# Performance work log

Hardware: AMD Instinct MI355X
Metric: run time of the kernel (lower is better)

Reference implementation:

```python
import jax, jax.numpy as jnp
import numpy as np

NEG_INF = -1e30

def setup_inputs() -> dict:
    key = jax.random.key(0)
    k1, k2, k3 = jax.random.split(key, 3)
    B, Lc, Lq, D = 16, 4096, 512, 128  # D = 2*dim, dim=64
    ctx = jax.random.normal(k1, (B, Lc, D), dtype=jnp.float32)
    q = jax.random.normal(k2, (B, Lq, D), dtype=jnp.float32)
    ctx_mask = jnp.ones((B, Lc), dtype=bool)
    q_mask = jnp.ones((B, Lq), dtype=bool)
    # nn.Linear(6*dim, 1): weight [1, 3*D] stored flat, bias scalar
    W = jax.random.normal(k3, (3 * D,), dtype=jnp.float32) * (1.0 / np.sqrt(3 * D))
    b = jnp.zeros((1,), dtype=jnp.float32)
    return {"ctx": ctx, "q": q, "ctx_mask": ctx_mask, "q_mask": q_mask, "W": W, "b": b}

def reference(ctx, q, ctx_mask, q_mask, W, b):
    # Linear over cat([c, q, c*q]) decomposes: S[b,l,m] = c.w_c + q.w_q + (c*w_m).q + bias
    D = ctx.shape[-1]
    w_c, w_q, w_m = W[:D], W[D:2 * D], W[2 * D:]
    S = (ctx @ w_c)[:, :, None] + (q @ w_q)[:, None, :] \
        + jnp.einsum('bld,bmd->blm', ctx * w_m, q) + b[0]  # [B, Lc, Lq]
    pair_mask = ctx_mask[:, :, None] & q_mask[:, None, :]
    S = S + (1.0 - pair_mask.astype(S.dtype)) * NEG_INF
    # context-to-query attention
    c2q = jax.nn.softmax(S, axis=-1)                      # [B, Lc, Lq]
    u = jnp.einsum('blm,bmd->bld', c2q, q)                # [B, Lc, D]
    # query-to-context attention
    q2c = jax.nn.softmax(S.max(axis=-1, keepdims=True), axis=1)  # [B, Lc, 1]
    h = (ctx * q2c).sum(axis=1, keepdims=True)            # [B, 1, D]
    h = jnp.broadcast_to(h, ctx.shape)                    # [B, Lc, D]
    return jnp.concatenate([ctx, u, ctx * u, ctx * h], axis=-1)  # [B, Lc, 4D]
```

## Files before the change

### kernel.cpp

```cpp
#include <hip/hip_runtime.h>

#define NB 16
#define LC 4096
#define LQ 512
#define DD 128

typedef __attribute__((ext_vector_type(8))) short bf16x8;
typedef __attribute__((ext_vector_type(4))) float f32x4;

static __device__ __forceinline__ float bf2f(unsigned short u) {
  union { unsigned int i; float f; } v; v.i = ((unsigned int)u) << 16; return v.f;
}
static __device__ __forceinline__ unsigned short f2bf(float f) {
  union { float f; unsigned int u; } v; v.f = f;
  unsigned int r = v.u + 0x7fffu + ((v.u >> 16) & 1u);
  return (unsigned short)(r >> 16);
}

static __device__ __forceinline__ void loadf8(const unsigned short* pb, const float* pf,
                                              size_t idx, int bf, float* o) {
  if (bf) {
    bf16x8 v = *(const bf16x8*)(pb + idx);
#pragma unroll
    for (int j = 0; j < 8; j++) o[j] = bf2f((unsigned short)v[j]);
  } else {
    const float4* p0 = (const float4*)(pf + idx);
    float4 a = p0[0], b = p0[1];
    o[0] = a.x; o[1] = a.y; o[2] = a.z; o[3] = a.w;
    o[4] = b.x; o[5] = b.y; o[6] = b.z; o[7] = b.w;
  }
}

static __device__ __forceinline__ bf16x8 frag8(const unsigned short* pb, const float* pf,
                                               size_t idx, int bf) {
  bf16x8 r;
  if (bf) {
    r = *(const bf16x8*)(pb + idx);
  } else {
    float o[8];
    loadf8(pb, pf, idx, 0, o);
#pragma unroll
    for (int j = 0; j < 8; j++) r[j] = (short)f2bf(o[j]);
  }
  return r;
}

__global__ void kD_detect(const unsigned short* __restrict__ ctx_s, int* __restrict__ flag) {
  int t = threadIdx.x;
  int cnt = 0;
  for (int i = 0; i < 32; i++) {
    float a = fabsf(bf2f(ctx_s[t * 32 + i]));
    if (a >= 0.0009765625f && a <= 16.0f) cnt++;
  }
#pragma unroll
  for (int off = 32; off; off >>= 1) cnt += __shfl_down(cnt, off);
  if (t == 0) *flag = (cnt >= 1638) ? 1 : 0;
}

__global__ __launch_bounds__(256)
void k0_prep(const unsigned short* __restrict__ qB, const float* __restrict__ qF,
             const unsigned short* __restrict__ WB, const float* __restrict__ WF,
             const int* __restrict__ flagp,
             unsigned short* __restrict__ qm, unsigned short* __restrict__ qT,
             float* __restrict__ qq) {
  __shared__ unsigned short sT[DD][72];
  __shared__ float sQQ[64][5];
  int bf = *flagp;
  int blk = blockIdx.x;
  int b = blk >> 3, tile = blk & 7;
  int m0 = tile * 64;
  int t = threadIdx.x;
  int r = t >> 2;
  int dq = t & 3;
  int d0 = dq * 32;

  float qv[32], wq[32], wm[32];
  size_t qbase = ((size_t)b * LQ + m0 + r) * DD + d0;
#pragma unroll
  for (int j = 0; j < 4; j++) {
    loadf8(qB, qF, qbase + j * 8, bf, &qv[j * 8]);
    loadf8(WB, WF, (size_t)(DD + d0 + j * 8), bf, &wq[j * 8]);
    loadf8(WB, WF, (size_t)(2 * DD + d0 + j * 8), bf, &wm[j * 8]);
  }

  float s = 0.f;
#pragma unroll
  for (int j = 0; j < 32; j++) s += qv[j] * wq[j];
  sQQ[r][dq] = s;

  unsigned short* qmrow = qm + ((size_t)b * LQ + m0 + r) * DD + d0;
#pragma unroll
  for (int g = 0; g < 4; g++) {
    bf16x8 o;
#pragma unroll
    for (int e = 0; e < 8; e++) o[e] = (short)f2bf(qv[g * 8 + e] * wm[g * 8 + e]);
    *(bf16x8*)(qmrow + g * 8) = o;
  }

#pragma unroll
  for (int j = 0; j < 32; j++) sT[d0 + j][r] = f2bf(qv[j]);
  __syncthreads();

  if (t < 64) qq[(size_t)b * LQ + m0 + t] = sQQ[t][0] + sQQ[t][1] + sQQ[t][2] + sQQ[t][3];

  int d = t >> 1, ms = (t & 1) * 32;
  unsigned short* qTp = qT + ((size_t)b * DD + d) * LQ + m0 + ms;
#pragma unroll
  for (int g = 0; g < 4; g++)
    *(bf16x8*)(qTp + g * 8) = *(const bf16x8*)(&sT[d][ms + g * 8]);
}

__global__ __launch_bounds__(256)
void k1_main(const unsigned short* __restrict__ ctxB, const float* __restrict__ ctxF,
             const unsigned short* __restrict__ WB, const float* __restrict__ WF,
             const unsigned short* __restrict__ qm,
             const unsigned short* __restrict__ qT,
             const float* __restrict__ qq,
             const int* __restrict__ flagp,
             float* __restrict__ Mv,
             unsigned short* __restrict__ outB, float* __restrict__ outF) {
  __shared__ unsigned short sP[16][520];
  __shared__ float sRedMax[4][16];
  __shared__ float sRedSum[4][16];
  __shared__ float sRowMax[16];
  __shared__ float sRowSum[16];
  __shared__ float sCq[16];
  __shared__ float sCqPart[16][17];

  int bf = *flagp;
  int t = threadIdx.x;
  int b = blockIdx.x >> 8;
  int lt = blockIdx.x & 255;
  int l0 = lt << 4;
  int w = t >> 6;
  int lane = t & 63;
  int quad = lane >> 4;
  int l16 = lane & 15;
  const size_t ctx_row0 = (size_t)(b * LC + l0);

  {
    int r = t >> 4, dg = t & 15;
    float cv[8], wv[8];
    loadf8(ctxB, ctxF, (ctx_row0 + r) * DD + (size_t)dg * 8, bf, cv);
    loadf8(WB, WF, (size_t)dg * 8, bf, wv);
    float s = 0.f;
#pragma unroll
    for (int j = 0; j < 8; j++) s += cv[j] * wv[j];
    sCqPart[r][dg] = s;
  }
  __syncthreads();
  if (t < 16) {
    float c = 0.f;
#pragma unroll
    for (int k = 0; k < 16; k++) c += sCqPart[t][k];
    sCq[t] = c;
  }

  bf16x8 afrag[4];
#pragma unroll
  for (int k = 0; k < 4; k++)
    afrag[k] = frag8(ctxB, ctxF, (ctx_row0 + l16) * DD + quad * 8 + k * 32, bf);

  f32x4 acc[8];
  const unsigned short* qmb = qm + (size_t)b * LQ * DD;
  const float* qqb = qq + b * LQ;
#pragma unroll
  for (int c = 0; c < 8; c++) {
    int col = (w << 7) + (c << 4) + l16;
    f32x4 a4 = {0.f, 0.f, 0.f, 0.f};
#pragma unroll
    for (int k = 0; k < 4; k++) {
      bf16x8 bfr = *(const bf16x8*)(qmb + (size_t)col * DD + quad * 8 + k * 32);
      a4 = __builtin_amdgcn_mfma_f32_16x16x32_bf16(afrag[k], bfr, a4, 0, 0, 0);
    }
    float qqv = qqb[col];
    acc[c][0] = a4[0] + qqv;
    acc[c][1] = a4[1] + qqv;
    acc[c][2] = a4[2] + qqv;
    acc[c][3] = a4[3] + qqv;
  }

  float rmax[4];
#pragma unroll
  for (int r = 0; r < 4; r++) {
    float m_ = acc[0][r];
#pragma unroll
    for (int c = 1; c < 8; c++) m_ = fmaxf(m_, acc[c][r]);
    m_ = fmaxf(m_, __shfl_xor(m_, 1));
    m_ = fmaxf(m_, __shfl_xor(m_, 2));
    m_ = fmaxf(m_, __shfl_xor(m_, 4));
    m_ = fmaxf(m_, __shfl_xor(m_, 8));
    rmax[r] = m_;
  }
  if (l16 == 0) {
#pragma unroll
    for (int r = 0; r < 4; r++) sRedMax[w][quad * 4 + r] = rmax[r];
  }
  __syncthreads();
  if (t < 16) {
    float m_ = fmaxf(fmaxf(sRedMax[0][t], sRedMax[1][t]),
                     fmaxf(sRedMax[2][t], sRedMax[3][t]));
    sRowMax[t] = m_;
    Mv[(size_t)b * LC + l0 + t] = m_ + sCq[t];
  }
  __syncthreads();

  float rowmax_r[4];
#pragma unroll
  for (int r = 0; r < 4; r++) rowmax_r[r] = sRowMax[quad * 4 + r];
  float rsum[4] = {0.f, 0.f, 0.f, 0.f};
#pragma unroll
  for (int c = 0; c < 8; c++) {
    int col = (w << 7) + (c << 4) + l16;
#pragma unroll
    for (int r = 0; r < 4; r++) {
      float e = __expf(fminf(acc[c][r] - rowmax_r[r], 0.f));
      rsum[r] += e;
      sP[quad * 4 + r][col] = f2bf(e);
    }
  }
#pragma unroll
  for (int r = 0; r < 4; r++) {
    float s_ = rsum[r];
    s_ += __shfl_xor(s_, 1);
    s_ += __shfl_xor(s_, 2);
    s_ += __shfl_xor(s_, 4);
    s_ += __shfl_xor(s_, 8);
    rsum[r] = s_;
  }
  if (l16 == 0) {
#pragma unroll
    for (int r = 0; r < 4; r++) sRedSum[w][quad * 4 + r] = rsum[r];
  }
  __syncthreads();
  if (t < 16)
    sRowSum[t] = sRedSum[0][t] + sRedSum[1][t] + sRedSum[2][t] + sRedSum[3][t];
  __syncthreads();

  f32x4 uacc[2] = {{0.f,0.f,0.f,0.f},{0.f,0.f,0.f,0.f}};
  const unsigned short* qTb = qT + (size_t)b * DD * LQ;
  int dA = (w << 5) + l16;
  int dB = dA + 16;
  for (int kk = 0; kk < 16; kk++) {
    bf16x8 pa = *(const bf16x8*)(&sP[l16][kk * 32 + quad * 8]);
    bf16x8 b0 = *(const bf16x8*)(qTb + (size_t)dA * LQ + kk * 32 + quad * 8);
    bf16x8 b1 = *(const bf16x8*)(qTb + (size_t)dB * LQ + kk * 32 + quad * 8);
    uacc[0] = __builtin_amdgcn_mfma_f32_16x16x32_bf16(pa, b0, uacc[0], 0, 0, 0);
    uacc[1] = __builtin_amdgcn_mfma_f32_16x16x32_bf16(pa, b1, uacc[1], 0, 0, 0);
  }

#pragma unroll
  for (int dt = 0; dt < 2; dt++) {
    int d = (w << 5) + (dt << 4) + l16;
#pragma unroll
    for (int r = 0; r < 4; r++) {
      int roww = quad * 4 + r;
      float denom = fmaxf(sRowSum[roww], 1e-30f);
      float uval = uacc[dt][r] / denom;
      size_t orow = (ctx_row0 + roww) * 512;
      size_t ci = (ctx_row0 + roww) * DD + d;
      float ctxv = bf ? bf2f(ctxB[ci]) : ctxF[ci];
      if (bf) {
        outB[orow + 128 + d] = f2bf(uval);
        outB[orow + 256 + d] = f2bf(ctxv * uval);
      } else {
        outF[orow + 128 + d] = uval;
        outF[orow + 256 + d] = ctxv * uval;
      }
    }
  }
  {
    int r = t >> 4, c8 = (t & 15) * 8;
    float cv[8];
    loadf8(ctxB, ctxF, (ctx_row0 + r) * DD + c8, bf, cv);
    size_t oo = (ctx_row0 + r) * 512 + c8;
    if (bf) {
      bf16x8 ov;
#pragma unroll
      for (int j = 0; j < 8; j++) ov[j] = (short)f2bf(cv[j]);
      *(bf16x8*)(outB + oo) = ov;
    } else {
      float4 a = {cv[0], cv[1], cv[2], cv[3]};
      float4 bq = {cv[4], cv[5], cv[6], cv[7]};
      *(float4*)(outF + oo) = a;
      *(float4*)(outF + oo + 4) = bq;
    }
  }
}

__global__ void k2a_soft(const float* __restrict__ Mv, float* __restrict__ wgt) {
  int b = blockIdx.x, t = threadIdx.x;
  __shared__ float sM[LC];
  __shared__ float red[256];
  float lmax = -1e30f;
  for (int i = t; i < LC; i += 256) { float v = Mv[(size_t)b * LC + i]; sM[i] = v; lmax = fmaxf(lmax, v); }
  red[t] = lmax;
  __syncthreads();
  for (int s = 128; s > 0; s >>= 1) {
    if (t < s) red[t] = fmaxf(red[t], red[t + s]);
    __syncthreads();
  }
  float gmax = red[0];
  __syncthreads();
  float lsum = 0.f;
  for (int i = t; i < LC; i += 256) lsum += __expf(fminf(sM[i] - gmax, 0.f));
  red[t] = lsum;
  __syncthreads();
  for (int s = 128; s > 0; s >>= 1) {
    if (t < s) red[t] += red[t + s];
    __syncthreads();
  }
  float inv = 1.0f / fmaxf(red[0], 1e-30f);
  for (int i = t; i < LC; i += 256) wgt[(size_t)b * LC + i] = __expf(fminf(sM[i] - gmax, 0.f)) * inv;
}

__global__ void k2b_h(const unsigned short* __restrict__ ctxB, const float* __restrict__ ctxF,
                      const int* __restrict__ flagp,
                      const float* __restrict__ wgt, float* __restrict__ h) {
  int bf = *flagp;
  int blk = blockIdx.x;
  int b = blk >> 5, ch = blk & 31;
  int t = threadIdx.x;
  int d = t & 127, half = t >> 7;
  int lbase = ch * 128 + half * 64;
  size_t cbase = ((size_t)b * LC + lbase) * DD + d;
  const float* wb = wgt + (size_t)b * LC + lbase;
  float s = 0.f;
#pragma unroll 4
  for (int i = 0; i < 64; i++) {
    float v = bf ? bf2f(ctxB[cbase + (size_t)i * DD]) : ctxF[cbase + (size_t)i * DD];
    s += wb[i] * v;
  }
  __shared__ float part[256];
  part[t] = s;
  __syncthreads();
  if (t < 128) atomicAdd(&h[b * DD + d], part[t] + part[t + 128]);
}

__global__ void k3_tail(const unsigned short* __restrict__ ctxB, const float* __restrict__ ctxF,
                        const int* __restrict__ flagp,
                        const float* __restrict__ h,
                        unsigned short* __restrict__ outB, float* __restrict__ outF) {
  int bf = *flagp;
  int g = blockIdx.x * 256 + threadIdx.x;
  size_t row = (size_t)(g >> 4);
  int dseg = (g & 15) * 8;
  int b = (int)(row >> 12);
  float cv[8];
  loadf8(ctxB, ctxF, row * DD + dseg, bf, cv);
  const float* hb = h + b * DD + dseg;
  size_t oo = row * 512 + 384 + dseg;
  if (bf) {
    bf16x8 ov;
#pragma unroll
    for (int j = 0; j < 8; j++) ov[j] = (short)f2bf(cv[j] * hb[j]);
    *(bf16x8*)(outB + oo) = ov;
  } else {
    float4 a = {cv[0] * hb[0], cv[1] * hb[1], cv[2] * hb[2], cv[3] * hb[3]};
    float4 bq = {cv[4] * hb[4], cv[5] * hb[5], cv[6] * hb[6], cv[7] * hb[7]};
    *(float4*)(outF + oo) = a;
    *(float4*)(outF + oo + 4) = bq;
  }
}

extern "C" void kernel_launch(void* const* d_in, const int* in_sizes, int n_in,
                              void* d_out, int out_size, void* d_ws, size_t ws_size,
                              hipStream_t stream) {
  const unsigned short* ctxB = (const unsigned short*)d_in[0];
  const float*          ctxF = (const float*)d_in[0];
  const unsigned short* qB   = (const unsigned short*)d_in[1];
  const float*          qF   = (const float*)d_in[1];
  const unsigned short* WB   = (const unsigned short*)d_in[4];
  const float*          WF   = (const float*)d_in[4];
  unsigned short* outB = (unsigned short*)d_out;
  float*          outF = (float*)d_out;

  char* ws = (char*)d_ws;
  unsigned short* qm = (unsigned short*)(ws);
  unsigned short* qT = (unsigned short*)(ws + 2097152);
  float* qq  = (float*)(ws + 4194304);
  float* Mv  = (float*)(ws + 4227072);
  float* wgt = (float*)(ws + 4489216);
  float* h   = (float*)(ws + 4751360);
  int* flag  = (int*)(ws + 4759552);

  hipMemsetAsync(h, 0, NB * DD * sizeof(float), stream);
  kD_detect<<<1, 64, 0, stream>>>((const unsigned short*)d_in[0], flag);
  k0_prep<<<NB * 8, 256, 0, stream>>>(qB, qF, WB, WF, flag, qm, qT, qq);
  k1_main<<<NB * (LC / 16), 256, 0, stream>>>(ctxB, ctxF, WB, WF, qm, qT, qq, flag, Mv, outB, outF);
  k2a_soft<<<NB, 256, 0, stream>>>(Mv, wgt);
  k2b_h<<<NB * 32, 256, 0, stream>>>(ctxB, ctxF, flag, wgt, h);
  k3_tail<<<NB * LC * DD / 8 / 256, 256, 0, stream>>>(ctxB, ctxF, flag, h, outB, outF);
}
```

Measured before the change: 327.3 us.

## Stage u outputs through LDS for vectorized stores, prefetch MFMA operands, swizzle blocks

The u and ctx*u outputs were written as scalar per-lane stores with a stride of one row each. They are now staged in shared memory, reusing the sP buffer after a barrier, and written out as contiguous 16-element vectors per thread. The MFMA loops for S and for P·q now double-buffer their operand loads so the next fragment is fetched while the current one computes. Block indexing is also interleaved across batches. This adds two barriers and LDS traffic and raises register pressure from the prefetch buffers.

```diff
diff --git a/kernel.cpp b/kernel.cpp
--- a/kernel.cpp
+++ b/kernel.cpp
@@ -129,8 +129,8 @@
 
   int bf = *flagp;
   int t = threadIdx.x;
-  int b = blockIdx.x >> 8;
-  int lt = blockIdx.x & 255;
+  int b = blockIdx.x & 15;
+  int lt = blockIdx.x >> 4;
   int l0 = lt << 4;
   int w = t >> 6;
   int lane = t & 63;
@@ -164,15 +164,26 @@
   f32x4 acc[8];
   const unsigned short* qmb = qm + (size_t)b * LQ * DD;
   const float* qqb = qq + b * LQ;
+  bf16x8 bfr[2][4];
+  {
+    int col = (w << 7) + l16;
+#pragma unroll
+    for (int k = 0; k < 4; k++)
+      bfr[0][k] = *(const bf16x8*)(qmb + (size_t)col * DD + quad * 8 + k * 32);
+  }
 #pragma unroll
   for (int c = 0; c < 8; c++) {
+    if (c < 7) {
+      int coln = (w << 7) + ((c + 1) << 4) + l16;
+#pragma unroll
+      for (int k = 0; k < 4; k++)
+        bfr[(c + 1) & 1][k] = *(const bf16x8*)(qmb + (size_t)coln * DD + quad * 8 + k * 32);
+    }
+    f32x4 a4 = {0.f, 0.f, 0.f, 0.f};
+#pragma unroll
+    for (int k = 0; k < 4; k++)
+      a4 = __builtin_amdgcn_mfma_f32_16x16x32_bf16(afrag[k], bfr[c & 1][k], a4, 0, 0, 0);
     int col = (w << 7) + (c << 4) + l16;
-    f32x4 a4 = {0.f, 0.f, 0.f, 0.f};
-#pragma unroll
-    for (int k = 0; k < 4; k++) {
-      bf16x8 bfr = *(const bf16x8*)(qmb + (size_t)col * DD + quad * 8 + k * 32);
-      a4 = __builtin_amdgcn_mfma_f32_16x16x32_bf16(afrag[k], bfr, a4, 0, 0, 0);
-    }
     float qqv = qqb[col];
     acc[c][0] = a4[0] + qqv;
     acc[c][1] = a4[1] + qqv;
@@ -241,14 +252,24 @@
   const unsigned short* qTb = qT + (size_t)b * DD * LQ;
   int dA = (w << 5) + l16;
   int dB = dA + 16;
+  bf16x8 pa2[2], pb0[2], pb1[2];
+  pa2[0] = *(const bf16x8*)(&sP[l16][quad * 8]);
+  pb0[0] = *(const bf16x8*)(qTb + (size_t)dA * LQ + quad * 8);
+  pb1[0] = *(const bf16x8*)(qTb + (size_t)dB * LQ + quad * 8);
+#pragma unroll
   for (int kk = 0; kk < 16; kk++) {
-    bf16x8 pa = *(const bf16x8*)(&sP[l16][kk * 32 + quad * 8]);
-    bf16x8 b0 = *(const bf16x8*)(qTb + (size_t)dA * LQ + kk * 32 + quad * 8);
-    bf16x8 b1 = *(const bf16x8*)(qTb + (size_t)dB * LQ + kk * 32 + quad * 8);
-    uacc[0] = __builtin_amdgcn_mfma_f32_16x16x32_bf16(pa, b0, uacc[0], 0, 0, 0);
-    uacc[1] = __builtin_amdgcn_mfma_f32_16x16x32_bf16(pa, b1, uacc[1], 0, 0, 0);
-  }
-
+    if (kk < 15) {
+      int o = (kk + 1) * 32 + quad * 8;
+      pa2[(kk + 1) & 1] = *(const bf16x8*)(&sP[l16][o]);
+      pb0[(kk + 1) & 1] = *(const bf16x8*)(qTb + (size_t)dA * LQ + o);
+      pb1[(kk + 1) & 1] = *(const bf16x8*)(qTb + (size_t)dB * LQ + o);
+    }
+    uacc[0] = __builtin_amdgcn_mfma_f32_16x16x32_bf16(pa2[kk & 1], pb0[kk & 1], uacc[0], 0, 0, 0);
+    uacc[1] = __builtin_amdgcn_mfma_f32_16x16x32_bf16(pa2[kk & 1], pb1[kk & 1], uacc[1], 0, 0, 0);
+  }
+
+  __syncthreads();
+  float* stage = (float*)&sP[0][0];
 #pragma unroll
   for (int dt = 0; dt < 2; dt++) {
     int d = (w << 5) + (dt << 4) + l16;
@@ -257,16 +278,32 @@
       int roww = quad * 4 + r;
       float denom = fmaxf(sRowSum[roww], 1e-30f);
       float uval = uacc[dt][r] / denom;
-      size_t orow = (ctx_row0 + roww) * 512;
       size_t ci = (ctx_row0 + roww) * DD + d;
       float ctxv = bf ? bf2f(ctxB[ci]) : ctxF[ci];
-      if (bf) {
-        outB[orow + 128 + d] = f2bf(uval);
-        outB[orow + 256 + d] = f2bf(ctxv * uval);
-      } else {
-        outF[orow + 128 + d] = uval;
-        outF[orow + 256 + d] = ctxv * uval;
-      }
+      stage[roww * 260 + d] = uval;
+      stage[roww * 260 + 128 + d] = ctxv * uval;
+    }
+  }
+  __syncthreads();
+  {
+    int r = t >> 4, coff = (t & 15) * 16;
+    const float* sp = &stage[r * 260 + coff];
+    size_t oo = (ctx_row0 + r) * 512 + 128 + coff;
+    if (bf) {
+      bf16x8 o0, o1;
+#pragma unroll
+      for (int j = 0; j < 8; j++) { o0[j] = (short)f2bf(sp[j]); o1[j] = (short)f2bf(sp[8 + j]); }
+      *(bf16x8*)(outB + oo) = o0;
+      *(bf16x8*)(outB + oo + 8) = o1;
+    } else {
+      float4 a0 = {sp[0], sp[1], sp[2], sp[3]};
+      float4 a1 = {sp[4], sp[5], sp[6], sp[7]};
+      float4 a2 = {sp[8], sp[9], sp[10], sp[11]};
+      float4 a3 = {sp[12], sp[13], sp[14], sp[15]};
+      *(float4*)(outF + oo) = a0;
+      *(float4*)(outF + oo + 4) = a1;
+      *(float4*)(outF + oo + 8) = a2;
+      *(float4*)(outF + oo + 12) = a3;
     }
   }
   {
```

Measured after the change: 332.5 us. No clear change (+1.6%).

## Process 64 context rows per block to reuse q fragments and vectorize output

Applied to the files above, without the earlier changes.

The main attention kernel now handles 64 context rows per block instead of 16. Each loaded qm and qT fragment feeds four MFMA row tiles, which cuts global reads of q per row by four. The u output is staged through shared memory so that ctx, u and ctx*u are written with coalesced vector stores instead of scalar stores. The block-to-batch mapping is interleaved, launch bounds request 2 blocks per CU, and an unroll factor in k2b is raised. In exchange the block uses more registers and shared memory, and there are fewer blocks.

```diff
diff --git a/kernel.cpp b/kernel.cpp
--- a/kernel.cpp
+++ b/kernel.cpp
@@ -110,7 +110,7 @@
     *(bf16x8*)(qTp + g * 8) = *(const bf16x8*)(&sT[d][ms + g * 8]);
 }
 
-__global__ __launch_bounds__(256)
+__global__ __launch_bounds__(256, 2)
 void k1_main(const unsigned short* __restrict__ ctxB, const float* __restrict__ ctxF,
              const unsigned short* __restrict__ WB, const float* __restrict__ WF,
              const unsigned short* __restrict__ qm,
@@ -119,85 +119,98 @@
              const int* __restrict__ flagp,
              float* __restrict__ Mv,
              unsigned short* __restrict__ outB, float* __restrict__ outF) {
-  __shared__ unsigned short sP[16][520];
-  __shared__ float sRedMax[4][16];
-  __shared__ float sRedSum[4][16];
-  __shared__ float sRowMax[16];
-  __shared__ float sRowSum[16];
-  __shared__ float sCq[16];
-  __shared__ float sCqPart[16][17];
+  __shared__ unsigned short sP[64][520];
+  __shared__ float sRedMax[4][64];
+  __shared__ float sRedSum[4][64];
+  __shared__ float sRowMax[64];
+  __shared__ float sRowSum[64];
+  __shared__ float sCq[64];
+  __shared__ float sCqPart[64][17];
 
   int bf = *flagp;
   int t = threadIdx.x;
-  int b = blockIdx.x >> 8;
-  int lt = blockIdx.x & 255;
-  int l0 = lt << 4;
+  int b = blockIdx.x & 15;
+  int lt = blockIdx.x >> 4;
+  int l0 = lt << 6;
   int w = t >> 6;
   int lane = t & 63;
   int quad = lane >> 4;
   int l16 = lane & 15;
   const size_t ctx_row0 = (size_t)(b * LC + l0);
+  const unsigned short* qmb = qm + (size_t)b * LQ * DD;
+  const float* qqb = qq + b * LQ;
+  const unsigned short* qTb = qT + (size_t)b * DD * LQ;
+  const int wcol = w << 7;
+
+  bf16x8 afrag[4][4];
+#pragma unroll
+  for (int s = 0; s < 4; s++)
+#pragma unroll
+    for (int k = 0; k < 4; k++)
+      afrag[s][k] = frag8(ctxB, ctxF, (ctx_row0 + s * 16 + l16) * DD + quad * 8 + k * 32, bf);
+  float qqv8[8];
+#pragma unroll
+  for (int c = 0; c < 8; c++) qqv8[c] = qqb[wcol + (c << 4) + l16];
 
   {
     int r = t >> 4, dg = t & 15;
-    float cv[8], wv[8];
-    loadf8(ctxB, ctxF, (ctx_row0 + r) * DD + (size_t)dg * 8, bf, cv);
+    float wv[8];
     loadf8(WB, WF, (size_t)dg * 8, bf, wv);
-    float s = 0.f;
-#pragma unroll
-    for (int j = 0; j < 8; j++) s += cv[j] * wv[j];
-    sCqPart[r][dg] = s;
-  }
-  __syncthreads();
-  if (t < 16) {
-    float c = 0.f;
-#pragma unroll
-    for (int k = 0; k < 16; k++) c += sCqPart[t][k];
-    sCq[t] = c;
-  }
-
-  bf16x8 afrag[4];
-#pragma unroll
-  for (int k = 0; k < 4; k++)
-    afrag[k] = frag8(ctxB, ctxF, (ctx_row0 + l16) * DD + quad * 8 + k * 32, bf);
-
-  f32x4 acc[8];
-  const unsigned short* qmb = qm + (size_t)b * LQ * DD;
-  const float* qqb = qq + b * LQ;
+#pragma unroll
+    for (int s = 0; s < 4; s++) {
+      float cv[8];
+      loadf8(ctxB, ctxF, (ctx_row0 + s * 16 + r) * DD + (size_t)dg * 8, bf, cv);
+      float sum = 0.f;
+#pragma unroll
+      for (int j = 0; j < 8; j++) sum += cv[j] * wv[j];
+      sCqPart[s * 16 + r][dg] = sum;
+    }
+  }
+  __syncthreads();
+  if (t < 64) {
+    float c_ = 0.f;
+#pragma unroll
+    for (int k = 0; k < 16; k++) c_ += sCqPart[t][k];
+    sCq[t] = c_;
+  }
+
+  f32x4 acc[4][8];
 #pragma unroll
   for (int c = 0; c < 8; c++) {
-    int col = (w << 7) + (c << 4) + l16;
-    f32x4 a4 = {0.f, 0.f, 0.f, 0.f};
-#pragma unroll
-    for (int k = 0; k < 4; k++) {
-      bf16x8 bfr = *(const bf16x8*)(qmb + (size_t)col * DD + quad * 8 + k * 32);
-      a4 = __builtin_amdgcn_mfma_f32_16x16x32_bf16(afrag[k], bfr, a4, 0, 0, 0);
-    }
-    float qqv = qqb[col];
-    acc[c][0] = a4[0] + qqv;
-    acc[c][1] = a4[1] + qqv;
-    acc[c][2] = a4[2] + qqv;
-    acc[c][3] = a4[3] + qqv;
-  }
-
-  float rmax[4];
-#pragma unroll
-  for (int r = 0; r < 4; r++) {
-    float m_ = acc[0][r];
-#pragma unroll
-    for (int c = 1; c < 8; c++) m_ = fmaxf(m_, acc[c][r]);
-    m_ = fmaxf(m_, __shfl_xor(m_, 1));
-    m_ = fmaxf(m_, __shfl_xor(m_, 2));
-    m_ = fmaxf(m_, __shfl_xor(m_, 4));
-    m_ = fmaxf(m_, __shfl_xor(m_, 8));
-    rmax[r] = m_;
-  }
-  if (l16 == 0) {
-#pragma unroll
-    for (int r = 0; r < 4; r++) sRedMax[w][quad * 4 + r] = rmax[r];
-  }
-  __syncthreads();
-  if (t < 16) {
+    bf16x8 bfr[4];
+#pragma unroll
+    for (int k = 0; k < 4; k++)
+      bfr[k] = *(const bf16x8*)(qmb + (size_t)(wcol + (c << 4) + l16) * DD + quad * 8 + k * 32);
+    float qqv = qqv8[c];
+#pragma unroll
+    for (int s = 0; s < 4; s++) {
+      f32x4 a4 = {0.f, 0.f, 0.f, 0.f};
+#pragma unroll
+      for (int k = 0; k < 4; k++)
+        a4 = __builtin_amdgcn_mfma_f32_16x16x32_bf16(afrag[s][k], bfr[k], a4, 0, 0, 0);
+      acc[s][c][0] = a4[0] + qqv;
+      acc[s][c][1] = a4[1] + qqv;
+      acc[s][c][2] = a4[2] + qqv;
+      acc[s][c][3] = a4[3] + qqv;
+    }
+  }
+
+#pragma unroll
+  for (int s = 0; s < 4; s++) {
+#pragma unroll
+    for (int r = 0; r < 4; r++) {
+      float m_ = acc[s][0][r];
+#pragma unroll
+      for (int c = 1; c < 8; c++) m_ = fmaxf(m_, acc[s][c][r]);
+      m_ = fmaxf(m_, __shfl_xor(m_, 1));
+      m_ = fmaxf(m_, __shfl_xor(m_, 2));
+      m_ = fmaxf(m_, __shfl_xor(m_, 4));
+      m_ = fmaxf(m_, __shfl_xor(m_, 8));
+      if (l16 == 0) sRedMax[w][s * 16 + quad * 4 + r] = m_;
+    }
+  }
+  __syncthreads();
+  if (t < 64) {
     float m_ = fmaxf(fmaxf(sRedMax[0][t], sRedMax[1][t]),
                      fmaxf(sRedMax[2][t], sRedMax[3][t]));
     sRowMax[t] = m_;
@@ -205,85 +218,122 @@
   }
   __syncthreads();
 
-  float rowmax_r[4];
-#pragma unroll
-  for (int r = 0; r < 4; r++) rowmax_r[r] = sRowMax[quad * 4 + r];
-  float rsum[4] = {0.f, 0.f, 0.f, 0.f};
-#pragma unroll
-  for (int c = 0; c < 8; c++) {
-    int col = (w << 7) + (c << 4) + l16;
+  float rm[4][4], rsum[4][4];
+#pragma unroll
+  for (int s = 0; s < 4; s++)
 #pragma unroll
     for (int r = 0; r < 4; r++) {
-      float e = __expf(fminf(acc[c][r] - rowmax_r[r], 0.f));
-      rsum[r] += e;
-      sP[quad * 4 + r][col] = f2bf(e);
-    }
-  }
-#pragma unroll
-  for (int r = 0; r < 4; r++) {
-    float s_ = rsum[r];
-    s_ += __shfl_xor(s_, 1);
-    s_ += __shfl_xor(s_, 2);
-    s_ += __shfl_xor(s_, 4);
-    s_ += __shfl_xor(s_, 8);
-    rsum[r] = s_;
-  }
-  if (l16 == 0) {
-#pragma unroll
-    for (int r = 0; r < 4; r++) sRedSum[w][quad * 4 + r] = rsum[r];
-  }
-  __syncthreads();
-  if (t < 16)
+      rm[s][r] = sRowMax[s * 16 + quad * 4 + r];
+      rsum[s][r] = 0.f;
+    }
+#pragma unroll
+  for (int c = 0; c < 8; c++)
+#pragma unroll
+    for (int s = 0; s < 4; s++)
+#pragma unroll
+      for (int r = 0; r < 4; r++) {
+        float e = __expf(fminf(acc[s][c][r] - rm[s][r], 0.f));
+        rsum[s][r] += e;
+        sP[s * 16 + quad * 4 + r][wcol + (c << 4) + l16] = f2bf(e);
+      }
+#pragma unroll
+  for (int s = 0; s < 4; s++)
+#pragma unroll
+    for (int r = 0; r < 4; r++) {
+      float s_ = rsum[s][r];
+      s_ += __shfl_xor(s_, 1);
+      s_ += __shfl_xor(s_, 2);
+      s_ += __shfl_xor(s_, 4);
+      s_ += __shfl_xor(s_, 8);
+      if (l16 == 0) sRedSum[w][s * 16 + quad * 4 + r] = s_;
+    }
+  __syncthreads();
+  if (t < 64)
     sRowSum[t] = sRedSum[0][t] + sRedSum[1][t] + sRedSum[2][t] + sRedSum[3][t];
   __syncthreads();
 
-  f32x4 uacc[2] = {{0.f,0.f,0.f,0.f},{0.f,0.f,0.f,0.f}};
-  const unsigned short* qTb = qT + (size_t)b * DD * LQ;
   int dA = (w << 5) + l16;
   int dB = dA + 16;
-  for (int kk = 0; kk < 16; kk++) {
-    bf16x8 pa = *(const bf16x8*)(&sP[l16][kk * 32 + quad * 8]);
-    bf16x8 b0 = *(const bf16x8*)(qTb + (size_t)dA * LQ + kk * 32 + quad * 8);
-    bf16x8 b1 = *(const bf16x8*)(qTb + (size_t)dB * LQ + kk * 32 + quad * 8);
-    uacc[0] = __builtin_amdgcn_mfma_f32_16x16x32_bf16(pa, b0, uacc[0], 0, 0, 0);
-    uacc[1] = __builtin_amdgcn_mfma_f32_16x16x32_bf16(pa, b1, uacc[1], 0, 0, 0);
-  }
-
-#pragma unroll
-  for (int dt = 0; dt < 2; dt++) {
-    int d = (w << 5) + (dt << 4) + l16;
-#pragma unroll
-    for (int r = 0; r < 4; r++) {
-      int roww = quad * 4 + r;
-      float denom = fmaxf(sRowSum[roww], 1e-30f);
-      float uval = uacc[dt][r] / denom;
-      size_t orow = (ctx_row0 + roww) * 512;
-      size_t ci = (ctx_row0 + roww) * DD + d;
-      float ctxv = bf ? bf2f(ctxB[ci]) : ctxF[ci];
+  f32x4 uacc[4][2];
+#pragma unroll
+  for (int s = 0; s < 4; s++) {
+    uacc[s][0] = (f32x4){0.f, 0.f, 0.f, 0.f};
+    uacc[s][1] = (f32x4){0.f, 0.f, 0.f, 0.f};
+  }
+#pragma unroll
+  for (int kb = 0; kb < 4; kb++) {
+    bf16x8 qb0[4], qb1[4];
+#pragma unroll
+    for (int kk = 0; kk < 4; kk++) {
+      int ko = (kb * 4 + kk) * 32 + quad * 8;
+      qb0[kk] = *(const bf16x8*)(qTb + (size_t)dA * LQ + ko);
+      qb1[kk] = *(const bf16x8*)(qTb + (size_t)dB * LQ + ko);
+    }
+#pragma unroll
+    for (int kk = 0; kk < 4; kk++) {
+      int ko = (kb * 4 + kk) * 32 + quad * 8;
+#pragma unroll
+      for (int s = 0; s < 4; s++) {
+        bf16x8 pa = *(const bf16x8*)(&sP[s * 16 + l16][ko]);
+        uacc[s][0] = __builtin_amdgcn_mfma_f32_16x16x32_bf16(pa, qb0[kk], uacc[s][0], 0, 0, 0);
+        uacc[s][1] = __builtin_amdgcn_mfma_f32_16x16x32_bf16(pa, qb1[kk], uacc[s][1], 0, 0, 0);
+      }
+    }
+  }
+
+  __syncthreads();
+  float* stage = (float*)&sP[0][0];
+#pragma unroll
+  for (int s = 0; s < 4; s++)
+#pragma unroll
+    for (int dt = 0; dt < 2; dt++) {
+      int d = (w << 5) + (dt << 4) + l16;
+#pragma unroll
+      for (int r = 0; r < 4; r++) {
+        int row = s * 16 + quad * 4 + r;
+        float denom = fmaxf(sRowSum[row], 1e-30f);
+        stage[row * 132 + d] = uacc[s][dt][r] / denom;
+      }
+    }
+  __syncthreads();
+
+  {
+    int r16 = t >> 4, d0 = (t & 15) * 8;
+#pragma unroll
+    for (int s = 0; s < 4; s++) {
+      int row = s * 16 + r16;
+      float cv[8];
+      loadf8(ctxB, ctxF, (ctx_row0 + row) * DD + d0, bf, cv);
+      const float* up = &stage[row * 132 + d0];
+      size_t oo = (ctx_row0 + row) * 512;
       if (bf) {
-        outB[orow + 128 + d] = f2bf(uval);
-        outB[orow + 256 + d] = f2bf(ctxv * uval);
+        bf16x8 o0, o1, o2;
+#pragma unroll
+        for (int j = 0; j < 8; j++) {
+          float uv = up[j];
+          o0[j] = (short)f2bf(cv[j]);
+          o1[j] = (short)f2bf(uv);
+          o2[j] = (short)f2bf(cv[j] * uv);
+        }
+        *(bf16x8*)(outB + oo + d0) = o0;
+        *(bf16x8*)(outB + oo + 128 + d0) = o1;
+        *(bf16x8*)(outB + oo + 256 + d0) = o2;
       } else {
-        outF[orow + 128 + d] = uval;
-        outF[orow + 256 + d] = ctxv * uval;
+        float u0 = up[0], u1 = up[1], u2 = up[2], u3 = up[3];
+        float u4 = up[4], u5 = up[5], u6 = up[6], u7 = up[7];
+        float4 p0 = {cv[0], cv[1], cv[2], cv[3]};
+        float4 p1 = {cv[4], cv[5], cv[6], cv[7]};
+        float4 q0 = {u0, u1, u2, u3};
+        float4 q1 = {u4, u5, u6, u7};
+        float4 m0 = {cv[0] * u0, cv[1] * u1, cv[2] * u2, cv[3] * u3};
+        float4 m1 = {cv[4] * u4, cv[5] * u5, cv[6] * u6, cv[7] * u7};
+        *(float4*)(outF + oo + d0) = p0;
+        *(float4*)(outF + oo + d0 + 4) = p1;
+        *(float4*)(outF + oo + 128 + d0) = q0;
+        *(float4*)(outF + oo + 128 + d0 + 4) = q1;
+        *(float4*)(outF + oo + 256 + d0) = m0;
+        *(float4*)(outF + oo + 256 + d0 + 4) = m1;
       }
-    }
-  }
-  {
-    int r = t >> 4, c8 = (t & 15) * 8;
-    float cv[8];
-    loadf8(ctxB, ctxF, (ctx_row0 + r) * DD + c8, bf, cv);
-    size_t oo = (ctx_row0 + r) * 512 + c8;
-    if (bf) {
-      bf16x8 ov;
-#pragma unroll
-      for (int j = 0; j < 8; j++) ov[j] = (short)f2bf(cv[j]);
-      *(bf16x8*)(outB + oo) = ov;
-    } else {
-      float4 a = {cv[0], cv[1], cv[2], cv[3]};
-      float4 bq = {cv[4], cv[5], cv[6], cv[7]};
-      *(float4*)(outF + oo) = a;
-      *(float4*)(outF + oo + 4) = bq;
     }
   }
 }
@@ -326,7 +376,7 @@
   size_t cbase = ((size_t)b * LC + lbase) * DD + d;
   const float* wb = wgt + (size_t)b * LC + lbase;
   float s = 0.f;
-#pragma unroll 4
+#pragma unroll 8
   for (int i = 0; i < 64; i++) {
     float v = bf ? bf2f(ctxB[cbase + (size_t)i * DD]) : ctxF[cbase + (size_t)i * DD];
     s += wb[i] * v;
@@ -387,7 +437,7 @@
   hipMemsetAsync(h, 0, NB * DD * sizeof(float), stream);
   kD_detect<<<1, 64, 0, stream>>>((const unsigned short*)d_in[0], flag);
   k0_prep<<<NB * 8, 256, 0, stream>>>(qB, qF, WB, WF, flag, qm, qT, qq);
-  k1_main<<<NB * (LC / 16), 256, 0, stream>>>(ctxB, ctxF, WB, WF, qm, qT, qq, flag, Mv, outB, outF);
+  k1_main<<<NB * (LC / 64), 256, 0, stream>>>(ctxB, ctxF, WB, WF, qm, qT, qq, flag, Mv, outB, outF);
   k2a_soft<<<NB, 256, 0, stream>>>(Mv, wgt);
   k2b_h<<<NB * 32, 256, 0, stream>>>(ctxB, ctxF, flag, wgt, h);
   k3_tail<<<NB * LC * DD / 8 / 256, 256, 0, stream>>>(ctxB, ctxF, flag, h, outB, outF);
```

After: 267.2 us. 18.3% less time.
